# Optimization experiments

Measured on AMD Instinct MI355X. Metric: run time of the kernel, lower is better.

## Reference

```python
import jax, jax.numpy as jnp
import numpy as np

EPS = 1e-7
N = 100000
E = 1600000
IN_DIM = 128
OUT_DIM = 128


def _norm(t):
    # clamped L2 norm over last dim, keepdims
    return jnp.clip(jnp.linalg.norm(t, axis=-1, keepdims=True), EPS, None)


def log_map_zero(x, c):
    sqrt_c = jnp.sqrt(c)
    xn = _norm(x)
    y = jnp.clip(sqrt_c * xn, None, 1.0 - 1e-5)
    return jnp.arctanh(y) * x / (sqrt_c * xn)


def exp_map_zero(v, c):
    sqrt_c = jnp.sqrt(c)
    vn = _norm(v)
    return jnp.tanh(sqrt_c * vn) * v / (sqrt_c * vn)


def setup_inputs() -> dict:
    key = jax.random.key(0)
    k1, k2, k3, k4 = jax.random.split(key, 4)
    x = 0.1 * jax.random.normal(k1, (N, IN_DIM), dtype=jnp.float32)  # inside ball
    edge_index = jax.random.randint(k2, (2, E), 0, N, dtype=jnp.int64)
    c = jnp.ones((), dtype=jnp.float32)
    # Xavier-uniform weight (out_dim, in_dim)
    limit = float(np.sqrt(6.0 / (IN_DIM + OUT_DIM)))
    weight = jax.random.uniform(k3, (OUT_DIM, IN_DIM), minval=-limit, maxval=limit, dtype=jnp.float32)
    bias = jnp.zeros((OUT_DIM,), dtype=jnp.float32)
    return {"x": x, "edge_index": edge_index, "c": c, "num_nodes": N,
            "weight": weight, "bias": bias}


def reference(x, edge_index, c, num_nodes, weight, bias):
    # 1. log-map all node features to tangent space at origin
    v = log_map_zero(x, c)  # (N, in_dim)
    src, dst = edge_index[0], edge_index[1]
    # 2. mean aggregation over neighbours (incl. self) via segment_sum
    agg = jax.ops.segment_sum(v[src], dst, num_segments=num_nodes) + v
    count = jax.ops.segment_sum(jnp.ones((src.shape[0],), dtype=v.dtype), dst,
                                num_segments=num_nodes) + 1.0
    v_agg = agg / jnp.clip(count, 1.0, None)[:, None]
    # 3. back to hyperbolic space, then hyperbolic linear
    x_hyp = exp_map_zero(v_agg, c)
    v2 = log_map_zero(x_hyp, c)
    out = v2 @ weight.T + bias
    return exp_map_zero(out, c)
```

## Files before the change

### kernel.cpp

```cpp
#include <hip/hip_runtime.h>
#include <math.h>

#define EPSF 1e-7f
#define YMAXF 0.99999f
#define WPITCH 136

#define NBUCK 256
#define PB_CHUNK 2048

typedef short bf16x8 __attribute__((ext_vector_type(8)));
typedef short bf16x4 __attribute__((ext_vector_type(4)));
typedef float f32x4  __attribute__((ext_vector_type(4)));

__device__ __forceinline__ float grp32_sum(float v) {
    v += __shfl_xor(v, 1);
    v += __shfl_xor(v, 2);
    v += __shfl_xor(v, 4);
    v += __shfl_xor(v, 8);
    v += __shfl_xor(v, 16);
    return v;
}

__device__ __forceinline__ short f2bf(float f) {
    unsigned u = __float_as_uint(f);
    unsigned r = (u + 0x7FFFu + ((u >> 16) & 1u)) >> 16;
    return (short)r;
}

__device__ __forceinline__ float bf2f(short u) {
    return __uint_as_float(((unsigned)(unsigned short)u) << 16);
}

__global__ void logmap_kernel(const float* __restrict__ x,
                              const float* __restrict__ c_ptr,
                              short* __restrict__ v_bf,
                              int N) {
    int gid = blockIdx.x * blockDim.x + threadIdx.x;
    int row = gid >> 5;
    if (row >= N) return;
    int lane = gid & 31;
    const float4 xv = ((const float4*)x)[(size_t)row * 32 + lane];
    float ss = xv.x * xv.x + xv.y * xv.y + xv.z * xv.z + xv.w * xv.w;
    ss = grp32_sum(ss);
    float sc = sqrtf(c_ptr[0]);
    float xn = fmaxf(sqrtf(ss), EPSF);
    float y = fminf(sc * xn, YMAXF);
    float s = atanhf(y) / (sc * xn);
    bf16x4 pk;
    pk[0] = f2bf(s * xv.x); pk[1] = f2bf(s * xv.y);
    pk[2] = f2bf(s * xv.z); pk[3] = f2bf(s * xv.w);
    *(bf16x4*)&v_bf[(size_t)row * 128 + lane * 4] = pk;
}

__global__ __launch_bounds__(256)
void bucket_count_kernel(const int* __restrict__ eidx_dst,
                         int* __restrict__ bucketCount, int E) {
    __shared__ int h[NBUCK];
    int tid = threadIdx.x;
    h[tid] = 0;
    __syncthreads();
    int per = (E + gridDim.x - 1) / gridDim.x;
    int start = blockIdx.x * per;
    int end = min(start + per, E);
    for (int i = start + tid; i < end; i += 256)
        atomicAdd(&h[eidx_dst[i] >> 9], 1);
    __syncthreads();
    if (h[tid]) atomicAdd(&bucketCount[tid], h[tid]);
}

__global__ __launch_bounds__(256)
void bucket_scan_kernel(const int* __restrict__ bucketCount,
                        int* __restrict__ bucket_base,
                        int* __restrict__ cursor) {
    __shared__ int part[256];
    int tid = threadIdx.x;
    int val = bucketCount[tid];
    part[tid] = val;
    __syncthreads();
    for (int off = 1; off < 256; off <<= 1) {
        int t = (tid >= off) ? part[tid - off] : 0;
        __syncthreads();
        part[tid] += t;
        __syncthreads();
    }
    int excl = part[tid] - val;
    bucket_base[tid] = excl;
    cursor[tid] = excl;
}

__global__ __launch_bounds__(256)
void bucket_scatter_kernel(const int* __restrict__ eidx,
                           int* __restrict__ cursor,
                           int* __restrict__ bucketed, int E) {
    __shared__ int hist[NBUCK];
    __shared__ int lstart[NBUCK];
    __shared__ int gbase[NBUCK];
    __shared__ int part[256];
    __shared__ int stage[PB_CHUNK];
    __shared__ unsigned char stageB[PB_CHUNK];

    int tid = threadIdx.x;
    int start = blockIdx.x * PB_CHUNK;
    int cnt = min(PB_CHUNK, E - start);
    hist[tid] = 0;
    __syncthreads();

    const int J = PB_CHUNK / 256;
    int myP[J], myB[J], myR[J];
    #pragma unroll
    for (int j = 0; j < J; ++j) {
        int idx = j * 256 + tid;
        myR[j] = -1;
        if (idx < cnt) {
            int e = start + idx;
            int d = eidx[E + e];
            int s = eidx[e];
            int b = d >> 9;
            myB[j] = b;
            myP[j] = ((d & 511) << 17) | s;
            myR[j] = atomicAdd(&hist[b], 1);
        }
    }
    __syncthreads();
    part[tid] = hist[tid];
    __syncthreads();
    for (int off = 1; off < 256; off <<= 1) {
        int t = (tid >= off) ? part[tid - off] : 0;
        __syncthreads();
        part[tid] += t;
        __syncthreads();
    }
    lstart[tid] = part[tid] - hist[tid];
    if (hist[tid]) gbase[tid] = atomicAdd(&cursor[tid], hist[tid]);
    __syncthreads();
    #pragma unroll
    for (int j = 0; j < J; ++j) {
        if (myR[j] >= 0) {
            int pos = lstart[myB[j]] + myR[j];
            stage[pos] = myP[j];
            stageB[pos] = (unsigned char)myB[j];
        }
    }
    __syncthreads();
    for (int i = tid; i < cnt; i += 256) {
        int b = stageB[i];
        bucketed[gbase[b] + (i - lstart[b])] = stage[i];
    }
}

__global__ __launch_bounds__(256)
void csr_kernel(const int* __restrict__ bucketed,
                const int* __restrict__ bucket_base,
                const int* __restrict__ cursor_post,
                int* __restrict__ offsets, int* __restrict__ deg,
                int* __restrict__ sorted_src, int N) {
    __shared__ int hist[512];
    __shared__ int pre[512];
    __shared__ int cur[512];
    __shared__ int part[256];
    int b = blockIdx.x;
    int tid = threadIdx.x;
    int start = bucket_base[b];
    int end = cursor_post[b];
    hist[tid] = 0;
    hist[tid + 256] = 0;
    __syncthreads();
    for (int i = start + tid; i < end; i += 256)
        atomicAdd(&hist[bucketed[i] >> 17], 1);
    __syncthreads();
    int a0 = hist[2 * tid], a1 = hist[2 * tid + 1];
    part[tid] = a0 + a1;
    __syncthreads();
    for (int off = 1; off < 256; off <<= 1) {
        int t = (tid >= off) ? part[tid - off] : 0;
        __syncthreads();
        part[tid] += t;
        __syncthreads();
    }
    int base2 = part[tid] - (a0 + a1);
    pre[2 * tid] = base2;
    pre[2 * tid + 1] = base2 + a0;
    cur[2 * tid] = base2;
    cur[2 * tid + 1] = base2 + a0;
    __syncthreads();
    int node0 = b << 9;
    for (int i = tid; i < 512; i += 256) {
        int node = node0 + i;
        if (node < N) { offsets[node] = start + pre[i]; deg[node] = hist[i]; }
    }
    for (int i = start + tid; i < end; i += 256) {
        int p = bucketed[i];
        int ld = p >> 17;
        int src = p & 0x1FFFF;
        int r = atomicAdd(&cur[ld], 1);
        sorted_src[start + r] = src;
    }
}

__global__ __launch_bounds__(256)
void gather_epilogue_kernel(const short* __restrict__ v_bf,
                            const int* __restrict__ sorted_src,
                            const int* __restrict__ offsets,
                            const int* __restrict__ deg,
                            const float* __restrict__ W,
                            const float* __restrict__ bias,
                            const float* __restrict__ c_ptr,
                            float* __restrict__ out,
                            int N, int tiles_per_block) {
    __shared__ short Wl[128 * WPITCH];
    __shared__ short v2l[16 * WPITCH];
    __shared__ float bias_s[128];
    __shared__ float outss[16][4];
    __shared__ float gscale[16];

    int tid = threadIdx.x;
    for (int i = tid; i < 4096; i += 256) {
        float4 w4 = ((const float4*)W)[i];
        int o = i >> 5;
        int k = (i & 31) * 4;
        bf16x4 w;
        w[0] = f2bf(w4.x); w[1] = f2bf(w4.y); w[2] = f2bf(w4.z); w[3] = f2bf(w4.w);
        *(bf16x4*)&Wl[o * WPITCH + k] = w;
    }
    if (tid < 128) bias_s[tid] = bias[tid];
    float sc = sqrtf(c_ptr[0]);
    __syncthreads();

    int wave = tid >> 6;
    int lane = tid & 63;
    int quad = lane >> 4;
    int l16  = lane & 15;
    int g  = tid >> 4;
    int gl = tid & 15;
    int n0 = wave * 32;
    float b0 = bias_s[n0 + l16];
    float b1 = bias_s[n0 + 16 + l16];

    for (int t = 0; t < tiles_per_block; ++t) {
        int row0 = (blockIdx.x * tiles_per_block + t) * 16;
        if (row0 >= N) break;
        int row = row0 + g;
        bool valid = (row < N);

        float acc[8];
        #pragma unroll
        for (int i = 0; i < 8; ++i) acc[i] = 0.0f;
        int start = 0, d = 0;
        if (valid) {
            start = offsets[row];
            d = deg[row];
            bf16x8 r0 = *(const bf16x8*)&v_bf[(size_t)row * 128 + gl * 8];
            #pragma unroll
            for (int i = 0; i < 8; ++i) acc[i] = bf2f(r0[i]);
        }
        for (int j = 0; j < d; j += 16) {
            int idx = j + gl;
            int batch = (idx < d) ? sorted_src[start + idx] : 0;
            int m = min(16, d - j);
            for (int jj = 0; jj < m; ++jj) {
                int src = __shfl(batch, (lane & 48) | jj);
                bf16x8 r = *(const bf16x8*)&v_bf[(size_t)src * 128 + gl * 8];
                #pragma unroll
                for (int i = 0; i < 8; ++i) acc[i] += bf2f(r[i]);
            }
        }
        float inv = 1.0f / (float)(d + 1);
        #pragma unroll
        for (int i = 0; i < 8; ++i) acc[i] *= inv;

        float ss = 0.0f;
        #pragma unroll
        for (int i = 0; i < 8; ++i) ss += acc[i] * acc[i];
        ss += __shfl_xor(ss, 1);
        ss += __shfl_xor(ss, 2);
        ss += __shfl_xor(ss, 4);
        ss += __shfl_xor(ss, 8);

        float vn  = sqrtf(ss);
        float vnc = fmaxf(vn, EPSF);
        float th  = tanhf(sc * vnc);
        float tt  = th / (sc * vnc);
        float hn  = fmaxf(th / sc, EPSF);
        float y2  = fminf(sc * hn, YMAXF);
        float s2  = atanhf(y2) / (sc * hn);
        float scale = s2 * tt;

        bf16x8 pk;
        #pragma unroll
        for (int i = 0; i < 8; ++i) pk[i] = f2bf(acc[i] * scale);
        *(bf16x8*)&v2l[g * WPITCH + gl * 8] = pk;
        __syncthreads();

        f32x4 acc0 = {b0, b0, b0, b0};
        f32x4 acc1 = {b1, b1, b1, b1};
        #pragma unroll
        for (int k0 = 0; k0 < 128; k0 += 32) {
            bf16x8 af  = *(const bf16x8*)&v2l[l16 * WPITCH + k0 + quad * 8];
            bf16x8 bf0 = *(const bf16x8*)&Wl[(n0 + l16) * WPITCH + k0 + quad * 8];
            bf16x8 bf1 = *(const bf16x8*)&Wl[(n0 + 16 + l16) * WPITCH + k0 + quad * 8];
            acc0 = __builtin_amdgcn_mfma_f32_16x16x32_bf16(af, bf0, acc0, 0, 0, 0);
            acc1 = __builtin_amdgcn_mfma_f32_16x16x32_bf16(af, bf1, acc1, 0, 0, 0);
        }

        float pss[4];
        #pragma unroll
        for (int r = 0; r < 4; ++r) {
            float vsum = acc0[r]*acc0[r] + acc1[r]*acc1[r];
            vsum += __shfl_xor(vsum, 1);
            vsum += __shfl_xor(vsum, 2);
            vsum += __shfl_xor(vsum, 4);
            vsum += __shfl_xor(vsum, 8);
            pss[r] = vsum;
        }
        if (l16 == 0) {
            #pragma unroll
            for (int r = 0; r < 4; ++r) outss[quad * 4 + r][wave] = pss[r];
        }
        __syncthreads();
        if (tid < 16) {
            float on  = sqrtf(outss[tid][0] + outss[tid][1] + outss[tid][2] + outss[tid][3]);
            float onc = fmaxf(on, EPSF);
            gscale[tid] = tanhf(sc * onc) / (sc * onc);
        }
        __syncthreads();
        #pragma unroll
        for (int r = 0; r < 4; ++r) {
            int orow = quad * 4 + r;
            if (row0 + orow < N) {
                float gsc = gscale[orow];
                size_t base = (size_t)(row0 + orow) * 128;
                out[base + n0 + l16]      = gsc * acc0[r];
                out[base + n0 + 16 + l16] = gsc * acc1[r];
            }
        }
        __syncthreads();
    }
}

extern "C" void kernel_launch(void* const* d_in, const int* in_sizes, int n_in,
                              void* d_out, int out_size, void* d_ws, size_t ws_size,
                              hipStream_t stream) {
    const float* x     = (const float*)d_in[0];
    const int*   eidx  = (const int*)d_in[1];
    const float* c_ptr = (const float*)d_in[2];
    const float* W     = (const float*)d_in[4];
    const float* bias  = (const float*)d_in[5];
    float* out = (float*)d_out;

    int N = in_sizes[0] / 128;
    int E = in_sizes[1] / 2;

    short* v_bf        = (short*)d_ws;
    int*   deg         = (int*)(v_bf + (size_t)N * 128);
    int*   offsets     = deg + N;
    int*   bucketCount = offsets + N;
    int*   bucket_base = bucketCount + NBUCK;
    int*   cursor      = bucket_base + NBUCK;
    int*   bucketed    = cursor + NBUCK;
    int*   sorted_src  = bucketed + E;

    hipMemsetAsync(bucketCount, 0, NBUCK * sizeof(int), stream);

    {
        long long threads = (long long)N * 32;
        int blocks = (int)((threads + 255) / 256);
        hipLaunchKernelGGL(logmap_kernel, dim3(blocks), dim3(256), 0, stream,
                           x, c_ptr, v_bf, N);
    }
    hipLaunchKernelGGL(bucket_count_kernel, dim3(256), dim3(256), 0, stream,
                       eidx + E, bucketCount, E);
    hipLaunchKernelGGL(bucket_scan_kernel, dim3(1), dim3(256), 0, stream,
                       bucketCount, bucket_base, cursor);
    {
        int blocks = (E + PB_CHUNK - 1) / PB_CHUNK;
        hipLaunchKernelGGL(bucket_scatter_kernel, dim3(blocks), dim3(256), 0, stream,
                           eidx, cursor, bucketed, E);
    }
    {
        int blocks = (N + 511) / 512;
        hipLaunchKernelGGL(csr_kernel, dim3(blocks), dim3(256), 0, stream,
                           bucketed, bucket_base, cursor, offsets, deg, sorted_src, N);
    }
    {
        const int TPB = 5;
        int numTiles = (N + 15) / 16;
        int blocks = (numTiles + TPB - 1) / TPB;
        hipLaunchKernelGGL(gather_epilogue_kernel, dim3(blocks), dim3(256), 0, stream,
                           v_bf, sorted_src, offsets, deg, W, bias, c_ptr, out, N, TPB);
    }
}
```

Baseline: 312.4 us.

## Split gather from GEMM epilogue, one wave per row, fold bucket scan into consumers

The fused gather+GEMM kernel becomes two kernels. A gather kernel assigns one 64-lane wave per node, each lane reading bf16 pairs, unrolled four neighbours at a time, and writes the post-log/exp scaled vector to a new bf16 buffer. A wave-independent MFMA epilogue then computes all 128 output columns per wave with no block barriers. The standalone bucket scan kernel is removed, and each scatter and CSR block recomputes the 256-entry prefix scan itself, with cursor now holding a relative offset. The aim is better memory-level parallelism in the gather and fewer barriers and launches, at the cost of an extra N×128 bf16 round trip through global memory and redundant scans.

New measurement: 346.6 us. +10.9%, slower.

```diff
diff --git a/kernel.cpp b/kernel.cpp
--- a/kernel.cpp
+++ b/kernel.cpp
@@ -10,6 +10,7 @@
 
 typedef short bf16x8 __attribute__((ext_vector_type(8)));
 typedef short bf16x4 __attribute__((ext_vector_type(4)));
+typedef short bf16x2 __attribute__((ext_vector_type(2)));
 typedef float f32x4  __attribute__((ext_vector_type(4)));
 
 __device__ __forceinline__ float grp32_sum(float v) {
@@ -69,27 +70,8 @@
 }
 
 __global__ __launch_bounds__(256)
-void bucket_scan_kernel(const int* __restrict__ bucketCount,
-                        int* __restrict__ bucket_base,
-                        int* __restrict__ cursor) {
-    __shared__ int part[256];
-    int tid = threadIdx.x;
-    int val = bucketCount[tid];
-    part[tid] = val;
-    __syncthreads();
-    for (int off = 1; off < 256; off <<= 1) {
-        int t = (tid >= off) ? part[tid - off] : 0;
-        __syncthreads();
-        part[tid] += t;
-        __syncthreads();
-    }
-    int excl = part[tid] - val;
-    bucket_base[tid] = excl;
-    cursor[tid] = excl;
-}
-
-__global__ __launch_bounds__(256)
 void bucket_scatter_kernel(const int* __restrict__ eidx,
+                           const int* __restrict__ bucketCount,
                            int* __restrict__ cursor,
                            int* __restrict__ bucketed, int E) {
     __shared__ int hist[NBUCK];
@@ -131,7 +113,18 @@
         __syncthreads();
     }
     lstart[tid] = part[tid] - hist[tid];
-    if (hist[tid]) gbase[tid] = atomicAdd(&cursor[tid], hist[tid]);
+    __syncthreads();
+    int bc = bucketCount[tid];
+    part[tid] = bc;
+    __syncthreads();
+    for (int off = 1; off < 256; off <<= 1) {
+        int t = (tid >= off) ? part[tid - off] : 0;
+        __syncthreads();
+        part[tid] += t;
+        __syncthreads();
+    }
+    int base = part[tid] - bc;
+    if (hist[tid]) gbase[tid] = base + atomicAdd(&cursor[tid], hist[tid]);
     __syncthreads();
     #pragma unroll
     for (int j = 0; j < J; ++j) {
@@ -150,21 +143,31 @@
 
 __global__ __launch_bounds__(256)
 void csr_kernel(const int* __restrict__ bucketed,
-                const int* __restrict__ bucket_base,
-                const int* __restrict__ cursor_post,
+                const int* __restrict__ bucketCount,
                 int* __restrict__ offsets, int* __restrict__ deg,
                 int* __restrict__ sorted_src, int N) {
     __shared__ int hist[512];
     __shared__ int pre[512];
     __shared__ int cur[512];
     __shared__ int part[256];
+    __shared__ int startEnd[2];
     int b = blockIdx.x;
     int tid = threadIdx.x;
-    int start = bucket_base[b];
-    int end = cursor_post[b];
+    int bc = bucketCount[tid];
+    part[tid] = bc;
+    __syncthreads();
+    for (int off = 1; off < 256; off <<= 1) {
+        int t = (tid >= off) ? part[tid - off] : 0;
+        __syncthreads();
+        part[tid] += t;
+        __syncthreads();
+    }
+    if (tid == b) { startEnd[0] = part[tid] - bc; startEnd[1] = part[tid]; }
     hist[tid] = 0;
     hist[tid + 256] = 0;
     __syncthreads();
+    int start = startEnd[0];
+    int end = startEnd[1];
     for (int i = start + tid; i < end; i += 256)
         atomicAdd(&hist[bucketed[i] >> 17], 1);
     __syncthreads();
@@ -198,20 +201,99 @@
 }
 
 __global__ __launch_bounds__(256)
-void gather_epilogue_kernel(const short* __restrict__ v_bf,
-                            const int* __restrict__ sorted_src,
-                            const int* __restrict__ offsets,
-                            const int* __restrict__ deg,
-                            const float* __restrict__ W,
-                            const float* __restrict__ bias,
-                            const float* __restrict__ c_ptr,
-                            float* __restrict__ out,
-                            int N, int tiles_per_block) {
+void gather_kernel(const short* __restrict__ v_bf,
+                   const int* __restrict__ sorted_src,
+                   const int* __restrict__ offsets,
+                   const int* __restrict__ deg,
+                   const float* __restrict__ c_ptr,
+                   short* __restrict__ v2_bf,
+                   int N) {
+    int row = (blockIdx.x * 256 + threadIdx.x) >> 6;
+    if (row >= N) return;
+    int lane = threadIdx.x & 63;
+    int start = offsets[row];
+    int d = deg[row];
+
+    bf16x2 sf = *(const bf16x2*)&v_bf[(size_t)row * 128 + lane * 2];
+    float a0 = bf2f(sf[0]);
+    float a1 = bf2f(sf[1]);
+
+    int j = 0;
+    for (; j + 64 <= d; j += 64) {
+        int batch = sorted_src[start + j + lane];
+        #pragma unroll
+        for (int jj = 0; jj < 64; jj += 4) {
+            int i0 = __shfl(batch, jj);
+            int i1 = __shfl(batch, jj + 1);
+            int i2 = __shfl(batch, jj + 2);
+            int i3 = __shfl(batch, jj + 3);
+            bf16x2 r0 = *(const bf16x2*)&v_bf[(size_t)i0 * 128 + lane * 2];
+            bf16x2 r1 = *(const bf16x2*)&v_bf[(size_t)i1 * 128 + lane * 2];
+            bf16x2 r2 = *(const bf16x2*)&v_bf[(size_t)i2 * 128 + lane * 2];
+            bf16x2 r3 = *(const bf16x2*)&v_bf[(size_t)i3 * 128 + lane * 2];
+            a0 += (bf2f(r0[0]) + bf2f(r1[0])) + (bf2f(r2[0]) + bf2f(r3[0]));
+            a1 += (bf2f(r0[1]) + bf2f(r1[1])) + (bf2f(r2[1]) + bf2f(r3[1]));
+        }
+    }
+    int m = d - j;
+    if (m > 0) {
+        int batch = (lane < m) ? sorted_src[start + j + lane] : 0;
+        int jj = 0;
+        for (; jj + 4 <= m; jj += 4) {
+            int i0 = __shfl(batch, jj);
+            int i1 = __shfl(batch, jj + 1);
+            int i2 = __shfl(batch, jj + 2);
+            int i3 = __shfl(batch, jj + 3);
+            bf16x2 r0 = *(const bf16x2*)&v_bf[(size_t)i0 * 128 + lane * 2];
+            bf16x2 r1 = *(const bf16x2*)&v_bf[(size_t)i1 * 128 + lane * 2];
+            bf16x2 r2 = *(const bf16x2*)&v_bf[(size_t)i2 * 128 + lane * 2];
+            bf16x2 r3 = *(const bf16x2*)&v_bf[(size_t)i3 * 128 + lane * 2];
+            a0 += (bf2f(r0[0]) + bf2f(r1[0])) + (bf2f(r2[0]) + bf2f(r3[0]));
+            a1 += (bf2f(r0[1]) + bf2f(r1[1])) + (bf2f(r2[1]) + bf2f(r3[1]));
+        }
+        for (; jj < m; ++jj) {
+            int s = __shfl(batch, jj);
+            bf16x2 r = *(const bf16x2*)&v_bf[(size_t)s * 128 + lane * 2];
+            a0 += bf2f(r[0]);
+            a1 += bf2f(r[1]);
+        }
+    }
+    float inv = 1.0f / (float)(d + 1);
+    a0 *= inv;
+    a1 *= inv;
+
+    float ss = a0 * a0 + a1 * a1;
+    ss += __shfl_xor(ss, 1);
+    ss += __shfl_xor(ss, 2);
+    ss += __shfl_xor(ss, 4);
+    ss += __shfl_xor(ss, 8);
+    ss += __shfl_xor(ss, 16);
+    ss += __shfl_xor(ss, 32);
+
+    float sc  = sqrtf(c_ptr[0]);
+    float vn  = sqrtf(ss);
+    float vnc = fmaxf(vn, EPSF);
+    float th  = tanhf(sc * vnc);
+    float tt  = th / (sc * vnc);
+    float hn  = fmaxf(th / sc, EPSF);
+    float y2  = fminf(sc * hn, YMAXF);
+    float s2  = atanhf(y2) / (sc * hn);
+    float scale = s2 * tt;
+
+    bf16x2 o;
+    o[0] = f2bf(a0 * scale);
+    o[1] = f2bf(a1 * scale);
+    *(bf16x2*)&v2_bf[(size_t)row * 128 + lane * 2] = o;
+}
+
+__global__ __launch_bounds__(256)
+void epilogue_kernel(const short* __restrict__ v2_bf,
+                     const float* __restrict__ W,
+                     const float* __restrict__ bias,
+                     const float* __restrict__ c_ptr,
+                     float* __restrict__ out,
+                     int N, int tiles_per_wave) {
     __shared__ short Wl[128 * WPITCH];
-    __shared__ short v2l[16 * WPITCH];
-    __shared__ float bias_s[128];
-    __shared__ float outss[16][4];
-    __shared__ float gscale[16];
 
     int tid = threadIdx.x;
     for (int i = tid; i < 4096; i += 256) {
@@ -222,118 +304,64 @@
         w[0] = f2bf(w4.x); w[1] = f2bf(w4.y); w[2] = f2bf(w4.z); w[3] = f2bf(w4.w);
         *(bf16x4*)&Wl[o * WPITCH + k] = w;
     }
-    if (tid < 128) bias_s[tid] = bias[tid];
-    float sc = sqrtf(c_ptr[0]);
     __syncthreads();
 
     int wave = tid >> 6;
     int lane = tid & 63;
     int quad = lane >> 4;
     int l16  = lane & 15;
-    int g  = tid >> 4;
-    int gl = tid & 15;
-    int n0 = wave * 32;
-    float b0 = bias_s[n0 + l16];
-    float b1 = bias_s[n0 + 16 + l16];
-
-    for (int t = 0; t < tiles_per_block; ++t) {
-        int row0 = (blockIdx.x * tiles_per_block + t) * 16;
-        if (row0 >= N) break;
-        int row = row0 + g;
-        bool valid = (row < N);
-
-        float acc[8];
+    float sc = sqrtf(c_ptr[0]);
+    float bcol[8];
+    #pragma unroll
+    for (int ct = 0; ct < 8; ++ct) bcol[ct] = bias[ct * 16 + l16];
+
+    int numTiles = (N + 15) / 16;
+    int tile0 = (blockIdx.x * 4 + wave) * tiles_per_wave;
+
+    for (int t = 0; t < tiles_per_wave; ++t) {
+        int tile = tile0 + t;
+        if (tile >= numTiles) break;
+        int row0 = tile * 16;
+        int rowA = min(row0 + l16, N - 1);
+
+        bf16x8 af[4];
         #pragma unroll
-        for (int i = 0; i < 8; ++i) acc[i] = 0.0f;
-        int start = 0, d = 0;
-        if (valid) {
-            start = offsets[row];
-            d = deg[row];
-            bf16x8 r0 = *(const bf16x8*)&v_bf[(size_t)row * 128 + gl * 8];
+        for (int k0 = 0; k0 < 4; ++k0)
+            af[k0] = *(const bf16x8*)&v2_bf[(size_t)rowA * 128 + k0 * 32 + quad * 8];
+
+        f32x4 acc[8];
+        #pragma unroll
+        for (int ct = 0; ct < 8; ++ct) {
+            float b = bcol[ct];
+            f32x4 a = {b, b, b, b};
             #pragma unroll
-            for (int i = 0; i < 8; ++i) acc[i] = bf2f(r0[i]);
-        }
-        for (int j = 0; j < d; j += 16) {
-            int idx = j + gl;
-            int batch = (idx < d) ? sorted_src[start + idx] : 0;
-            int m = min(16, d - j);
-            for (int jj = 0; jj < m; ++jj) {
-                int src = __shfl(batch, (lane & 48) | jj);
-                bf16x8 r = *(const bf16x8*)&v_bf[(size_t)src * 128 + gl * 8];
-                #pragma unroll
-                for (int i = 0; i < 8; ++i) acc[i] += bf2f(r[i]);
+            for (int k0 = 0; k0 < 4; ++k0) {
+                bf16x8 bf = *(const bf16x8*)&Wl[(ct * 16 + l16) * WPITCH + k0 * 32 + quad * 8];
+                a = __builtin_amdgcn_mfma_f32_16x16x32_bf16(af[k0], bf, a, 0, 0, 0);
             }
-        }
-        float inv = 1.0f / (float)(d + 1);
-        #pragma unroll
-        for (int i = 0; i < 8; ++i) acc[i] *= inv;
-
-        float ss = 0.0f;
-        #pragma unroll
-        for (int i = 0; i < 8; ++i) ss += acc[i] * acc[i];
-        ss += __shfl_xor(ss, 1);
-        ss += __shfl_xor(ss, 2);
-        ss += __shfl_xor(ss, 4);
-        ss += __shfl_xor(ss, 8);
-
-        float vn  = sqrtf(ss);
-        float vnc = fmaxf(vn, EPSF);
-        float th  = tanhf(sc * vnc);
-        float tt  = th / (sc * vnc);
-        float hn  = fmaxf(th / sc, EPSF);
-        float y2  = fminf(sc * hn, YMAXF);
-        float s2  = atanhf(y2) / (sc * hn);
-        float scale = s2 * tt;
-
-        bf16x8 pk;
-        #pragma unroll
-        for (int i = 0; i < 8; ++i) pk[i] = f2bf(acc[i] * scale);
-        *(bf16x8*)&v2l[g * WPITCH + gl * 8] = pk;
-        __syncthreads();
-
-        f32x4 acc0 = {b0, b0, b0, b0};
-        f32x4 acc1 = {b1, b1, b1, b1};
-        #pragma unroll
-        for (int k0 = 0; k0 < 128; k0 += 32) {
-            bf16x8 af  = *(const bf16x8*)&v2l[l16 * WPITCH + k0 + quad * 8];
-            bf16x8 bf0 = *(const bf16x8*)&Wl[(n0 + l16) * WPITCH + k0 + quad * 8];
-            bf16x8 bf1 = *(const bf16x8*)&Wl[(n0 + 16 + l16) * WPITCH + k0 + quad * 8];
-            acc0 = __builtin_amdgcn_mfma_f32_16x16x32_bf16(af, bf0, acc0, 0, 0, 0);
-            acc1 = __builtin_amdgcn_mfma_f32_16x16x32_bf16(af, bf1, acc1, 0, 0, 0);
-        }
-
-        float pss[4];
+            acc[ct] = a;
+        }
+
         #pragma unroll
         for (int r = 0; r < 4; ++r) {
-            float vsum = acc0[r]*acc0[r] + acc1[r]*acc1[r];
-            vsum += __shfl_xor(vsum, 1);
-            vsum += __shfl_xor(vsum, 2);
-            vsum += __shfl_xor(vsum, 4);
-            vsum += __shfl_xor(vsum, 8);
-            pss[r] = vsum;
-        }
-        if (l16 == 0) {
+            float ssum = 0.0f;
             #pragma unroll
-            for (int r = 0; r < 4; ++r) outss[quad * 4 + r][wave] = pss[r];
-        }
-        __syncthreads();
-        if (tid < 16) {
-            float on  = sqrtf(outss[tid][0] + outss[tid][1] + outss[tid][2] + outss[tid][3]);
+            for (int ct = 0; ct < 8; ++ct) ssum += acc[ct][r] * acc[ct][r];
+            ssum += __shfl_xor(ssum, 1);
+            ssum += __shfl_xor(ssum, 2);
+            ssum += __shfl_xor(ssum, 4);
+            ssum += __shfl_xor(ssum, 8);
+            float on  = sqrtf(ssum);
             float onc = fmaxf(on, EPSF);
-            gscale[tid] = tanhf(sc * onc) / (sc * onc);
-        }
-        __syncthreads();
-        #pragma unroll
-        for (int r = 0; r < 4; ++r) {
-            int orow = quad * 4 + r;
-            if (row0 + orow < N) {
-                float gsc = gscale[orow];
-                size_t base = (size_t)(row0 + orow) * 128;
-                out[base + n0 + l16]      = gsc * acc0[r];
-                out[base + n0 + 16 + l16] = gsc * acc1[r];
+            float g   = tanhf(sc * onc) / (sc * onc);
+            int row = row0 + quad * 4 + r;
+            if (row < N) {
+                size_t base = (size_t)row * 128;
+                #pragma unroll
+                for (int ct = 0; ct < 8; ++ct)
+                    out[base + ct * 16 + l16] = g * acc[ct][r];
             }
         }
-        __syncthreads();
     }
 }
 
@@ -351,15 +379,15 @@
     int E = in_sizes[1] / 2;
 
     short* v_bf        = (short*)d_ws;
-    int*   deg         = (int*)(v_bf + (size_t)N * 128);
+    short* v2_bf       = v_bf + (size_t)N * 128;
+    int*   deg         = (int*)(v2_bf + (size_t)N * 128);
     int*   offsets     = deg + N;
     int*   bucketCount = offsets + N;
-    int*   bucket_base = bucketCount + NBUCK;
-    int*   cursor      = bucket_base + NBUCK;
+    int*   cursor      = bucketCount + NBUCK;
     int*   bucketed    = cursor + NBUCK;
     int*   sorted_src  = bucketed + E;
 
-    hipMemsetAsync(bucketCount, 0, NBUCK * sizeof(int), stream);
+    hipMemsetAsync(bucketCount, 0, 2 * NBUCK * sizeof(int), stream);
 
     {
         long long threads = (long long)N * 32;
@@ -367,25 +395,28 @@
         hipLaunchKernelGGL(logmap_kernel, dim3(blocks), dim3(256), 0, stream,
                            x, c_ptr, v_bf, N);
     }
-    hipLaunchKernelGGL(bucket_count_kernel, dim3(256), dim3(256), 0, stream,
+    hipLaunchKernelGGL(bucket_count_kernel, dim3(512), dim3(256), 0, stream,
                        eidx + E, bucketCount, E);
-    hipLaunchKernelGGL(bucket_scan_kernel, dim3(1), dim3(256), 0, stream,
-                       bucketCount, bucket_base, cursor);
     {
         int blocks = (E + PB_CHUNK - 1) / PB_CHUNK;
         hipLaunchKernelGGL(bucket_scatter_kernel, dim3(blocks), dim3(256), 0, stream,
-                           eidx, cursor, bucketed, E);
+                           eidx, bucketCount, cursor, bucketed, E);
     }
     {
         int blocks = (N + 511) / 512;
         hipLaunchKernelGGL(csr_kernel, dim3(blocks), dim3(256), 0, stream,
-                           bucketed, bucket_base, cursor, offsets, deg, sorted_src, N);
+                           bucketed, bucketCount, offsets, deg, sorted_src, N);
     }
     {
-        const int TPB = 5;
+        int blocks = (N + 3) / 4;
+        hipLaunchKernelGGL(gather_kernel, dim3(blocks), dim3(256), 0, stream,
+                           v_bf, sorted_src, offsets, deg, c_ptr, v2_bf, N);
+    }
+    {
+        const int TPW = 4;
         int numTiles = (N + 15) / 16;
-        int blocks = (numTiles + TPB - 1) / TPB;
-        hipLaunchKernelGGL(gather_epilogue_kernel, dim3(blocks), dim3(256), 0, stream,
-                           v_bf, sorted_src, offsets, deg, W, bias, c_ptr, out, N, TPB);
-    }
-}
+        int blocks = (numTiles + 4 * TPW - 1) / (4 * TPW);
+        hipLaunchKernelGGL(epilogue_kernel, dim3(blocks), dim3(256), 0, stream,
+                           v2_bf, W, bias, c_ptr, out, N, TPW);
+    }
+}
```
